# Optimization experiments

Hardware: AMD Instinct MI355X
Metric: run time of the kernel (lower is better)

The kernel has to match this reference:

```python
import jax, jax.numpy as jnp
import numpy as np

N_NODES = 100000
N_EDGES = 1200000
N_FEAT = 128
EMB = 64
N_CLASSES = 2
N_GRAPHS = 256


def _glorot(key, shape):
    lim = float(np.sqrt(6.0 / (shape[0] + shape[1])))
    return jax.random.uniform(key, shape, minval=-lim, maxval=lim, dtype=jnp.float32)


def setup_inputs() -> dict:
    key = jax.random.key(0)
    ks = jax.random.split(key, 12)
    x = jax.random.normal(ks[0], (N_NODES, N_FEAT), dtype=jnp.float32)
    edge_index = jax.random.randint(ks[1], (2, N_EDGES), 0, N_NODES, dtype=jnp.int32)
    batch_index = jnp.sort(jax.random.randint(ks[2], (N_NODES,), 0, N_GRAPHS, dtype=jnp.int32))
    return {
        "x": x,
        "edge_index": edge_index,
        "batch_index": batch_index,
        "W0": _glorot(ks[3], (N_FEAT, EMB)), "b0": jnp.zeros((EMB,), jnp.float32),
        "W1": _glorot(ks[4], (EMB, EMB)),   "b1": jnp.zeros((EMB,), jnp.float32),
        "W2": _glorot(ks[5], (EMB, EMB)),   "b2": jnp.zeros((EMB,), jnp.float32),
        "W3": _glorot(ks[6], (EMB, EMB)),   "b3": jnp.zeros((EMB,), jnp.float32),
        "Wout": _glorot(ks[7], (2 * EMB, N_CLASSES)),
        "bout": jnp.zeros((N_CLASSES,), jnp.float32),
    }


def _gcn_conv(x, W, b, src, dst, norm, n):
    # PyG GCNConv: out[i] = sum_{j->i} norm_ij * (x[j] @ W) + b
    h = x @ W                                   # [N, D]
    agg = jax.ops.segment_sum(h[src] * norm[:, None], dst, num_segments=n)
    return agg + b


def reference(x, edge_index, batch_index, W0, b0, W1, b1, W2, b2, W3, b3, Wout, bout):
    n = x.shape[0]
    # add self-loops (GCNConv default)
    loops = jnp.arange(n, dtype=edge_index.dtype)
    src = jnp.concatenate([edge_index[0], loops])
    dst = jnp.concatenate([edge_index[1], loops])
    # symmetric normalization: deg computed on target index with unit weights
    deg = jax.ops.segment_sum(jnp.ones_like(src, dtype=x.dtype), dst, num_segments=n)
    dinv = jnp.where(deg > 0, jax.lax.rsqrt(deg), 0.0)
    norm = dinv[src] * dinv[dst]                # [E+N]

    h = jnp.tanh(_gcn_conv(x, W0, b0, src, dst, norm, n))
    h = jnp.tanh(_gcn_conv(h, W1, b1, src, dst, norm, n))
    h = jnp.tanh(_gcn_conv(h, W2, b2, src, dst, norm, n))
    h = jnp.tanh(_gcn_conv(h, W3, b3, src, dst, norm, n))

    # global max + mean pool per graph
    counts = jax.ops.segment_sum(jnp.ones((n,), x.dtype), batch_index, num_segments=N_GRAPHS)
    gsum = jax.ops.segment_sum(h, batch_index, num_segments=N_GRAPHS)
    gmean = gsum / jnp.maximum(counts, 1.0)[:, None]
    gmax = jax.ops.segment_max(h, batch_index, num_segments=N_GRAPHS)
    pooled = jnp.concatenate([gmax, gmean], axis=1)  # [G, 2*EMB]
    return pooled @ Wout + bout
```

## Files before the change

### kernel.cpp

```cpp
#include <hip/hip_runtime.h>
#include <hip/hip_bf16.h>
#include <hip/hip_fp16.h>
#include <math.h>

#define N_NODES   100000
#define N_EDGES   1200000
#define N_FEAT    128
#define EMB       64
#define N_GRAPHS  256

#define SCAN_ITEMS 1024
#define NB_SCAN    98


__global__ void k_count(const int* __restrict__ dst, int* __restrict__ cnt) {
    int e = blockIdx.x * 256 + threadIdx.x;
    if (e < N_EDGES) atomicAdd(&cnt[dst[e]], 1);
}

__global__ __launch_bounds__(256) void k_scan1(const int* __restrict__ cnt,
                                               int* __restrict__ rowp,
                                               int* __restrict__ bsum) {
    __shared__ int ts[256];
    int t = threadIdx.x;
    int base = blockIdx.x * SCAN_ITEMS + t * 4;
    int v[4];
#pragma unroll
    for (int i = 0; i < 4; i++) {
        int idx = base + i;
        v[i] = (idx < N_NODES) ? ((cnt[idx] + 3) & ~3) : 0;
    }
    int s = v[0] + v[1] + v[2] + v[3];
    ts[t] = s;
    __syncthreads();
    for (int off = 1; off < 256; off <<= 1) {
        int x = (t >= off) ? ts[t - off] : 0;
        __syncthreads();
        ts[t] += x;
        __syncthreads();
    }
    int run = (t > 0) ? ts[t - 1] : 0;
#pragma unroll
    for (int i = 0; i < 4; i++) {
        run += v[i];
        int idx = base + i;
        if (idx < N_NODES) rowp[1 + idx] = run;
    }
    if (t == 255) bsum[blockIdx.x] = ts[255];
}

__global__ __launch_bounds__(384) void k_scan2g(int* __restrict__ bsum,
                                                const int* __restrict__ batch,
                                                int* __restrict__ gptr) {
    __shared__ int ts[128];
    int t = threadIdx.x;
    int gv = 0;
    if (t >= 128) {
        int g = t - 128;
        int lo = 0, hi = N_NODES;
        while (lo < hi) {
            int mid = (lo + hi) >> 1;
            if (batch[mid] < g) lo = mid + 1; else hi = mid;
        }
        gv = lo;
    }
    if (t < 128) ts[t] = (t < NB_SCAN) ? bsum[t] : 0;
    __syncthreads();
    for (int off = 1; off < 128; off <<= 1) {
        int x = (t < 128 && t >= off) ? ts[t - off] : 0;
        __syncthreads();
        if (t < 128) ts[t] += x;
        __syncthreads();
    }
    if (t < 128) {
        int excl = (t > 0) ? ts[t - 1] : 0;
        if (t < NB_SCAN) bsum[t] = excl;
    } else {
        gptr[t - 128] = gv;
        if (t == 128) gptr[N_GRAPHS] = N_NODES;
    }
}

__global__ void k_scan3f(int* __restrict__ rowp, const int* __restrict__ bsum,
                         const int* __restrict__ cnt, float* __restrict__ dinv,
                         int* __restrict__ fillp) {
    int idx = blockIdx.x * 256 + threadIdx.x;
    if (idx >= N_NODES) return;
    int val = rowp[1 + idx] + bsum[idx >> 10];
    rowp[1 + idx] = val;
    if (idx + 1 < N_NODES) fillp[idx + 1] = val;
    dinv[idx] = rsqrtf((float)(cnt[idx] + 1));
    if (idx == 0) { rowp[0] = 0; fillp[0] = 0; }
}

__global__ void k_fill(const int* __restrict__ src, const int* __restrict__ dst,
                       int* __restrict__ fillp, int* __restrict__ ev) {
    int e = blockIdx.x * 256 + threadIdx.x;
    if (e >= N_EDGES) return;
    int s = src[e], d = dst[e];
    int p = atomicAdd(&fillp[d], 1);
    ev[p] = s;
}

template <int K>
__global__ __launch_bounds__(256) void k_gemm(const float* __restrict__ X,
                                              const float* __restrict__ W,
                                              const float* __restrict__ dinv,
                                              __half* __restrict__ Hh) {
    __shared__ float xs[64][17];
    __shared__ float ws[16][64];
    int t = threadIdx.x;
    int tx = t & 15;
    int ty = t >> 4;
    int row0 = blockIdx.x * 64;
    float acc[4][4] = {};
    for (int k0 = 0; k0 < K; k0 += 16) {
        {
            int r = t >> 2;
            int kk = (t & 3) * 4;
            int gr = row0 + r;
            float4 v = (gr < N_NODES)
                           ? *(const float4*)(X + (size_t)gr * K + k0 + kk)
                           : make_float4(0.f, 0.f, 0.f, 0.f);
            xs[r][kk + 0] = v.x; xs[r][kk + 1] = v.y;
            xs[r][kk + 2] = v.z; xs[r][kk + 3] = v.w;
        }
        {
            int kr = t >> 4;
            int c4 = (t & 15) * 4;
            float4 v = *(const float4*)(W + (size_t)(k0 + kr) * 64 + c4);
            *(float4*)&ws[kr][c4] = v;
        }
        __syncthreads();
#pragma unroll
        for (int k = 0; k < 16; ++k) {
            float xv[4], wv[4];
#pragma unroll
            for (int i = 0; i < 4; i++) xv[i] = xs[ty * 4 + i][k];
#pragma unroll
            for (int j = 0; j < 4; j++) wv[j] = ws[k][tx * 4 + j];
#pragma unroll
            for (int i = 0; i < 4; i++)
#pragma unroll
                for (int j = 0; j < 4; j++) acc[i][j] += xv[i] * wv[j];
        }
        __syncthreads();
    }
#pragma unroll
    for (int i = 0; i < 4; i++) {
        int gr = row0 + ty * 4 + i;
        if (gr < N_NODES) {
            float dv = dinv[gr];
            __half tmp[4];
            tmp[0] = __float2half_rn(acc[i][0] * dv);
            tmp[1] = __float2half_rn(acc[i][1] * dv);
            tmp[2] = __float2half_rn(acc[i][2] * dv);
            tmp[3] = __float2half_rn(acc[i][3] * dv);
            *(uint2*)(Hh + (size_t)gr * 64 + tx * 4) = *(uint2*)tmp;
        }
    }
}

__device__ __forceinline__ float2 h2f2(uint d) {
    union { uint u; __half2 h; } cv; cv.u = d;
    return make_float2(__half2float(cv.h.x), __half2float(cv.h.y));
}
__device__ __forceinline__ float fast_tanh(float x) {
    float e = __expf(2.f * x);
    return 1.f - 2.f / (e + 1.f);
}

template <bool MV, bool SCALE_OUT, typename OutT>
__global__ __launch_bounds__(256) void k_agg(const int* __restrict__ rowp,
                                             const int* __restrict__ cnt,
                                             const int* __restrict__ ev,
                                             const __half* __restrict__ X,
                                             const float* __restrict__ dinv,
                                             const float* __restrict__ W,
                                             const float* __restrict__ bias,
                                             OutT* __restrict__ out) {
    __shared__ float4 WQ[32][32];
    __shared__ float2 vbuf[4][2][32];
    int t = threadIdx.x;
    if (MV) {
        for (int id = t; id < 1024; id += 256) {
            int m = id >> 5, c = id & 31;
            float2 a = *(const float2*)(W + (size_t)(2 * m) * 64 + 2 * c);
            float2 b = *(const float2*)(W + (size_t)(2 * m + 1) * 64 + 2 * c);
            WQ[m][c] = make_float4(a.x, a.y, b.x, b.y);
        }
    }
    int w = t >> 6;
    int lane = t & 63;
    int half = lane >> 5;
    int c = lane & 31;
    uint c4 = (uint)c << 2;
    int wid = blockIdx.x * 4 + w;
    int n0 = wid * 2;
    int n = n0 + half;

    int pA = rowp[n0], pB = rowp[n0 + 1];
    int remA = cnt[n0], remB = cnt[n0 + 1];
    int ebase = half ? pB : pA;
    int rem   = half ? remB : remA;
    int maxrem = max(remA, remB);
    int minrem4 = min(remA, remB) & ~3;
    const char* Xb = (const char*)X;
    const int* ep = ev + ebase;

    float ax, ay;
    {
        uint d = *(const uint*)(Xb + (((uint)n) << 7) + c4);
        float2 f = h2f2(d);
        ax = f.x; ay = f.y;
    }
    int k = 0;
    if (minrem4 > 0) {
        int4 e4 = *(const int4*)ep;
        for (; k < minrem4; k += 4) {
            int4 nx = *(const int4*)(ep + k + 4);
            int idx[4] = {e4.x, e4.y, e4.z, e4.w};
            uint d[4];
#pragma unroll
            for (int u = 0; u < 4; ++u)
                d[u] = *(const uint*)(Xb + (((uint)idx[u]) << 7) + c4);
#pragma unroll
            for (int u = 0; u < 4; ++u) {
                float2 f = h2f2(d[u]);
                ax += f.x; ay += f.y;
            }
            e4 = nx;
        }
    }
    for (; k < maxrem; k += 4) {
        int4 e4 = *(const int4*)(ep + k);
        int idx[4] = {e4.x, e4.y, e4.z, e4.w};
        uint d[4];
#pragma unroll
        for (int u = 0; u < 4; ++u) {
            bool valid = (k + u) < rem;
            int s = valid ? idx[u] : 0;
            d[u] = *(const uint*)(Xb + (((uint)s) << 7) + c4);
        }
#pragma unroll
        for (int u = 0; u < 4; ++u) {
            bool valid = (k + u) < rem;
            float2 f = h2f2(valid ? d[u] : 0u);
            ax += f.x; ay += f.y;
        }
    }
    float di = dinv[n];
    ax *= di; ay *= di;

    float ox, oy;
    if (MV) {
        vbuf[w][half][c] = make_float2(ax, ay);
        __syncthreads();
        float2 b2 = *(const float2*)(bias + 2 * c);
        ox = b2.x; oy = b2.y;
#pragma unroll
        for (int m = 0; m < 32; ++m) {
            float2 v2 = vbuf[w][half][m];
            float4 w4 = WQ[m][c];
            ox += v2.x * w4.x + v2.y * w4.z;
            oy += v2.x * w4.y + v2.y * w4.w;
        }
    } else {
        float2 b2 = *(const float2*)(bias + 2 * c);
        ox = ax + b2.x; oy = ay + b2.y;
    }
    float hx = fast_tanh(ox);
    float hy = fast_tanh(oy);
    size_t obase = (size_t)n * 64 + 2 * c;
    if (SCALE_OUT) {
        *(__half2*)((__half*)out + obase) = __floats2half2_rn(hx * di, hy * di);
    } else {
        *(float2*)((float*)out + obase) = make_float2(hx, hy);
    }
}

__global__ __launch_bounds__(256) void k_pool(const float* __restrict__ A,
                                              const int* __restrict__ gptr,
                                              const float* __restrict__ Wout,
                                              const float* __restrict__ bout,
                                              float* __restrict__ out) {
    __shared__ float ssum[4][64];
    __shared__ float smax[4][64];
    int g = blockIdx.x;
    int t = threadIdx.x;
    int w = t >> 6, lane = t & 63;
    int start = gptr[g], end = gptr[g + 1];
    float s = 0.f, m = -INFINITY;
    for (int n = start + w; n < end; n += 4) {
        float v = A[(size_t)n * 64 + lane];
        s += v;
        m = fmaxf(m, v);
    }
    ssum[w][lane] = s;
    smax[w][lane] = m;
    __syncthreads();
    if (w == 0) {
        float st = ssum[0][lane] + ssum[1][lane] + ssum[2][lane] + ssum[3][lane];
        float mt = fmaxf(fmaxf(smax[0][lane], smax[1][lane]),
                         fmaxf(smax[2][lane], smax[3][lane]));
        int cntg = end - start;
        float mean = st / fmaxf((float)cntg, 1.0f);
        float p0 = mt * Wout[lane * 2 + 0] + mean * Wout[(64 + lane) * 2 + 0];
        float p1 = mt * Wout[lane * 2 + 1] + mean * Wout[(64 + lane) * 2 + 1];
#pragma unroll
        for (int off = 32; off >= 1; off >>= 1) {
            p0 += __shfl_down(p0, off);
            p1 += __shfl_down(p1, off);
        }
        if (lane == 0) {
            out[g * 2 + 0] = p0 + bout[0];
            out[g * 2 + 1] = p1 + bout[1];
        }
    }
}


extern "C" void kernel_launch(void* const* d_in, const int* in_sizes, int n_in,
                              void* d_out, int out_size, void* d_ws, size_t ws_size,
                              hipStream_t stream) {
    const float* x     = (const float*)d_in[0];
    const int*   eidx  = (const int*)d_in[1];
    const int*   batch = (const int*)d_in[2];
    const float* W0 = (const float*)d_in[3];  const float* b0 = (const float*)d_in[4];
    const float* W1 = (const float*)d_in[5];  const float* b1 = (const float*)d_in[6];
    const float* W2 = (const float*)d_in[7];  const float* b2 = (const float*)d_in[8];
    const float* W3 = (const float*)d_in[9];  const float* b3 = (const float*)d_in[10];
    const float* Wout = (const float*)d_in[11];
    const float* bout = (const float*)d_in[12];
    float* out = (float*)d_out;

    const int* esrc = eidx;
    const int* edst = eidx + N_EDGES;

    char* base = (char*)d_ws;
    size_t off = 0;
    auto carve = [&](size_t bytes) {
        void* p = base + off;
        off = (off + bytes + 255) & ~(size_t)255;
        return p;
    };
    float*  Af    = (float*)carve((size_t)N_NODES * 64 * 4);
    __half* Hh    = (__half*)carve((size_t)N_NODES * 64 * 2);
    __half* Ah    = (__half*)carve((size_t)N_NODES * 64 * 2);
    int*    ev    = (int*)carve(((size_t)N_EDGES + 3 * N_NODES + 256) * 4);
    int*    rowp  = (int*)carve((size_t)(N_NODES + 1) * 4);
    int*    fillp = (int*)carve((size_t)N_NODES * 4);
    int*    cnt   = (int*)carve((size_t)N_NODES * 4);
    float*  dinv  = (float*)carve((size_t)N_NODES * 4);
    int*    bsum  = (int*)carve((size_t)NB_SCAN * 4);
    int*    gptr  = (int*)carve((size_t)(N_GRAPHS + 1) * 4);
    (void)ws_size; (void)n_in; (void)in_sizes; (void)out_size;

    const int nBlkN = (N_NODES + 255) / 256;
    const int nBlkE = (N_EDGES + 255) / 256;

    hipMemsetAsync(cnt, 0, (size_t)N_NODES * 4, stream);
    hipLaunchKernelGGL(k_count,  dim3(nBlkE), dim3(256), 0, stream, edst, cnt);
    hipLaunchKernelGGL(k_scan1,  dim3(NB_SCAN), dim3(256), 0, stream, cnt, rowp, bsum);
    hipLaunchKernelGGL(k_scan2g, dim3(1), dim3(384), 0, stream, bsum, batch, gptr);
    hipLaunchKernelGGL(k_scan3f, dim3(nBlkN), dim3(256), 0, stream, rowp, bsum, cnt, dinv, fillp);
    hipLaunchKernelGGL(k_fill,   dim3(nBlkE), dim3(256), 0, stream, esrc, edst, fillp, ev);

    const int nBlkGemm = (N_NODES + 63) / 64;
    const int nBlkAgg  = N_NODES / 8;

    hipLaunchKernelGGL(k_gemm<128>, dim3(nBlkGemm), dim3(256), 0, stream, x, W0, dinv, Hh);
    hipLaunchKernelGGL((k_agg<false, true, __half>), dim3(nBlkAgg), dim3(256), 0, stream,
                       rowp, cnt, ev, Hh, dinv, (const float*)nullptr, b0, Ah);
    hipLaunchKernelGGL((k_agg<true, true, __half>), dim3(nBlkAgg), dim3(256), 0, stream,
                       rowp, cnt, ev, Ah, dinv, W1, b1, Hh);
    hipLaunchKernelGGL((k_agg<true, true, __half>), dim3(nBlkAgg), dim3(256), 0, stream,
                       rowp, cnt, ev, Hh, dinv, W2, b2, Ah);
    hipLaunchKernelGGL((k_agg<true, false, float>), dim3(nBlkAgg), dim3(256), 0, stream,
                       rowp, cnt, ev, Ah, dinv, W3, b3, Af);

    hipLaunchKernelGGL(k_pool, dim3(N_GRAPHS), dim3(256), 0, stream, Af, gptr, Wout, bout, out);
}
```

Baseline: 492.5 us.

## Partition edge count and fill atomics by destination range per XCD

The count and fill kernels become grid-stride loops over 1024 blocks, split into 8 groups by blockIdx&7. Each group handles only edges whose destination falls in its 1/8 node range. The aim is to keep each range's atomics on one XCD's L2 (assuming blocks are assigned to XCDs round-robin), so the atomics stay local instead of bouncing between chiplets. In exchange, every group reads the full dst array, which multiplies index reads by eight.

After: 469.3 us. -4.7%, faster.

```diff
diff --git a/kernel.cpp b/kernel.cpp
--- a/kernel.cpp
+++ b/kernel.cpp
@@ -12,10 +12,20 @@
 #define SCAN_ITEMS 1024
 #define NB_SCAN    98
 
-
-__global__ void k_count(const int* __restrict__ dst, int* __restrict__ cnt) {
-    int e = blockIdx.x * 256 + threadIdx.x;
-    if (e < N_EDGES) atomicAdd(&cnt[dst[e]], 1);
+#define NXCD      8
+#define RNG       (N_NODES / NXCD)
+#define GRP_BLKS  128
+
+
+__global__ __launch_bounds__(256) void k_count(const int* __restrict__ dst,
+                                               int* __restrict__ cnt) {
+    int g = blockIdx.x & 7;
+    int lo = g * RNG, hi = lo + RNG;
+    for (int e = (blockIdx.x >> 3) * 256 + threadIdx.x; e < N_EDGES;
+         e += GRP_BLKS * 256) {
+        int d = dst[e];
+        if (d >= lo && d < hi) atomicAdd(&cnt[d], 1);
+    }
 }
 
 __global__ __launch_bounds__(256) void k_scan1(const int* __restrict__ cnt,
@@ -93,13 +103,20 @@
     if (idx == 0) { rowp[0] = 0; fillp[0] = 0; }
 }
 
-__global__ void k_fill(const int* __restrict__ src, const int* __restrict__ dst,
-                       int* __restrict__ fillp, int* __restrict__ ev) {
-    int e = blockIdx.x * 256 + threadIdx.x;
-    if (e >= N_EDGES) return;
-    int s = src[e], d = dst[e];
-    int p = atomicAdd(&fillp[d], 1);
-    ev[p] = s;
+__global__ __launch_bounds__(256) void k_fill(const int* __restrict__ src,
+                                              const int* __restrict__ dst,
+                                              int* __restrict__ fillp,
+                                              int* __restrict__ ev) {
+    int g = blockIdx.x & 7;
+    int lo = g * RNG, hi = lo + RNG;
+    for (int e = (blockIdx.x >> 3) * 256 + threadIdx.x; e < N_EDGES;
+         e += GRP_BLKS * 256) {
+        int d = dst[e];
+        if (d >= lo && d < hi) {
+            int p = atomicAdd(&fillp[d], 1);
+            ev[p] = src[e];
+        }
+    }
 }
 
 template <int K>
@@ -357,14 +374,13 @@
     (void)ws_size; (void)n_in; (void)in_sizes; (void)out_size;
 
     const int nBlkN = (N_NODES + 255) / 256;
-    const int nBlkE = (N_EDGES + 255) / 256;
 
     hipMemsetAsync(cnt, 0, (size_t)N_NODES * 4, stream);
-    hipLaunchKernelGGL(k_count,  dim3(nBlkE), dim3(256), 0, stream, edst, cnt);
+    hipLaunchKernelGGL(k_count,  dim3(NXCD * GRP_BLKS), dim3(256), 0, stream, edst, cnt);
     hipLaunchKernelGGL(k_scan1,  dim3(NB_SCAN), dim3(256), 0, stream, cnt, rowp, bsum);
     hipLaunchKernelGGL(k_scan2g, dim3(1), dim3(384), 0, stream, bsum, batch, gptr);
     hipLaunchKernelGGL(k_scan3f, dim3(nBlkN), dim3(256), 0, stream, rowp, bsum, cnt, dinv, fillp);
-    hipLaunchKernelGGL(k_fill,   dim3(nBlkE), dim3(256), 0, stream, esrc, edst, fillp, ev);
+    hipLaunchKernelGGL(k_fill,   dim3(NXCD * GRP_BLKS), dim3(256), 0, stream, esrc, edst, fillp, ev);
 
     const int nBlkGemm = (N_NODES + 63) / 64;
     const int nBlkAgg  = N_NODES / 8;
```
